# Performance work log

Measured on AMD Instinct MI355X. Metric: run time of the kernel, lower is better.

Reference implementation:

```python
import jax, jax.numpy as jnp
import numpy as np

N_NODES = 50000
N_EDGES = 800000
F_DIM = 64
AVG_D_LOG = 2.833  # avg_d['log'] ~ log(avg_degree + 1)
EPS_STD = 1e-5     # PNA std aggregator epsilon
EPS_BN = 1e-5      # BatchNorm1d epsilon


def setup_inputs() -> dict:
    key = jax.random.key(0)
    k = jax.random.split(key, 5)
    h = jax.random.normal(k[0], (N_NODES, F_DIM), dtype=jnp.float32)
    src = jax.random.randint(k[1], (N_EDGES,), 0, N_NODES)
    dst = jax.random.randint(k[2], (N_EDGES,), 0, N_NODES)
    # posttrans: single Linear(12*F, F) (posttrans_layers=1, last_activation='none')
    W = jax.random.normal(k[3], (12 * F_DIM, F_DIM), dtype=jnp.float32) * 0.02
    b = jnp.zeros((F_DIM,), dtype=jnp.float32)
    gamma = jnp.ones((F_DIM,), dtype=jnp.float32)
    beta = jnp.zeros((F_DIM,), dtype=jnp.float32)
    return {"h": h, "src": src, "dst": dst, "W": W, "b": b, "gamma": gamma, "beta": beta}


def reference(h, src, dst, W, b, gamma, beta):
    N = h.shape[0]
    m = h[src]  # [E, F] messages: copy_u
    ones = jnp.ones((src.shape[0],), dtype=h.dtype)
    deg = jax.ops.segment_sum(ones, dst, num_segments=N)            # [N]
    s = jax.ops.segment_sum(m, dst, num_segments=N)                 # [N, F]
    s2 = jax.ops.segment_sum(m * m, dst, num_segments=N)            # [N, F]
    mx = jax.ops.segment_max(m, dst, num_segments=N)                # [N, F]
    mn = jax.ops.segment_min(m, dst, num_segments=N)                # [N, F]

    degc = jnp.maximum(deg, 1.0)[:, None]
    mean = s / degc
    var = jax.nn.relu(s2 / degc - mean * mean)
    std = jnp.sqrt(var + EPS_STD)

    # aggregator concat (dim=1): [mean | max | min | std] -> [N, 4F]
    agg = jnp.concatenate([mean, mx, mn, std], axis=1)
    has = (deg > 0)[:, None]
    agg = jnp.where(has, agg, 0.0)  # DGL zero-fills zero-in-degree nodes

    logD = jnp.log(deg + 1.0)[:, None]
    amp = agg * (logD / AVG_D_LOG)
    att = agg * jnp.where(has, AVG_D_LOG / jnp.maximum(logD, 1e-12), 0.0)

    # scaler concat: [identity | amplification | attenuation] -> [N, 12F]
    x = jnp.concatenate([agg, amp, att], axis=1)

    # posttrans linear
    x = x @ W + b

    # BatchNorm1d (training-mode batch statistics)
    mu = jnp.mean(x, axis=0)
    v = jnp.var(x, axis=0)
    x = gamma * (x - mu) / jnp.sqrt(v + EPS_BN) + beta

    x = jax.nn.relu(x)
    x = h + x  # residual (in_dim == out_dim)
    # dropout p=0.0 -> identity
    return x
```

## Files before the change

### kernel.cpp

```cpp
#include <hip/hip_runtime.h>
#include <hip/hip_bf16.h>

#define NND 50000
#define NED 800000
#define FD 64
#define PADW 64
#define MPAD2 50176
#define NBLK 196
#define NEBLK 3125
#define NXCD 8
#define NPX 6250
#define AVGDL 2.833f

typedef __attribute__((ext_vector_type(8))) short short8;
typedef __attribute__((ext_vector_type(4))) float floatx4;

__global__ __launch_bounds__(256) void prep(const float* __restrict__ W,
                                            __hip_bfloat16* __restrict__ Wf,
                                            int* __restrict__ deg,
                                            float* __restrict__ gsum,
                                            float* __restrict__ gsumsq,
                                            __hip_bfloat16* __restrict__ aggb) {
    int i = blockIdx.x * 256 + threadIdx.x;
    if (i < NND) deg[i] = 0;
    if (i < 64) { gsum[i] = 0.f; gsumsq[i] = 0.f; }
    if (i < (MPAD2 - NND) * 128) ((unsigned int*)(aggb + (size_t)NND * 256))[i] = 0u;
    if (i < 8 * 12 * 64 * 8) {
        int e = i & 7;
        int l = (i >> 3) & 63;
        int st = i >> 9;
        int t = st % 12, s5 = st / 12;
        int k = 32 * s5 + (l >> 4) * 8 + e;
        int col = 16 * t + (l & 15);
        int g = col >> 6, jj = col & 63;
        Wf[i] = __float2bfloat16(W[(g * 256 + k) * FD + jj]);
    }
}

__global__ __launch_bounds__(256) void fill_csr(const int* __restrict__ src,
                                                const int* __restrict__ dst,
                                                int* __restrict__ deg,
                                                int* __restrict__ csr) {
    int g = blockIdx.x & (NXCD - 1);
    int e = (blockIdx.x >> 3) * 256 + threadIdx.x;
    if (e < NED) {
        int d = dst[e];
        if ((unsigned)(d - g * NPX) < (unsigned)NPX) {
            int slot = atomicAdd(&deg[d], 1);
            if (slot < PADW) csr[d * PADW + slot] = src[e];
        }
    }
}

__global__ __launch_bounds__(256) void aggregate(
    const float* __restrict__ h, const int* __restrict__ deg,
    const int* __restrict__ csr, __hip_bfloat16* __restrict__ aggb,
    float* __restrict__ c1, float* __restrict__ c2) {
    int wid = blockIdx.x * 4 + (threadIdx.x >> 6);
    int lane = threadIdx.x & 63;
    if (wid >= NND) return;
    int d = deg[wid];
    if (d > PADW) d = PADW;
    float s = 0.f, s2 = 0.f, mx = -INFINITY, mn = INFINITY;
    if (d > 0) {
        const int* row_idx = csr + wid * PADW;
        int myidx = row_idx[lane < d ? lane : d - 1];
        for (int j = 0; j < d; j += 8) {
            float vv[8];
            #pragma unroll
            for (int q = 0; q < 8; ++q) {
                int jj = j + q;
                int jc = jj < d ? jj : d - 1;
                int ii = __shfl(myidx, jc);
                vv[q] = h[(size_t)ii * FD + lane];
            }
            #pragma unroll
            for (int q = 0; q < 8; ++q) {
                bool ok = (j + q) < d;
                float v = ok ? vv[q] : 0.f;
                s += v; s2 += v * v;
                mx = fmaxf(mx, ok ? vv[q] : -INFINITY);
                mn = fminf(mn, ok ? vv[q] : INFINITY);
            }
        }
    }
    float mean = 0.f, maxv = 0.f, minv = 0.f, stdv = 0.f, cc1 = 0.f, cc2 = 0.f;
    if (d > 0) {
        float degf = (float)d;
        mean = s / degf;
        float var = fmaxf(s2 / degf - mean * mean, 0.f);
        stdv = sqrtf(var + 1e-5f);
        maxv = mx; minv = mn;
        float logD = logf(degf + 1.f);
        cc1 = logD / AVGDL;
        cc2 = AVGDL / fmaxf(logD, 1e-12f);
    }
    __hip_bfloat16* row = aggb + (size_t)wid * 256;
    row[lane]       = __float2bfloat16(mean);
    row[64 + lane]  = __float2bfloat16(maxv);
    row[128 + lane] = __float2bfloat16(minv);
    row[192 + lane] = __float2bfloat16(stdv);
    if (lane == 0) { c1[wid] = cc1; c2[wid] = cc2; }
}

__global__ __launch_bounds__(512) void gemm_kernel(
    const __hip_bfloat16* __restrict__ aggb, const __hip_bfloat16* __restrict__ Wf,
    const float* __restrict__ c1, const float* __restrict__ c2,
    const float* __restrict__ bias,
    float* __restrict__ x, float* __restrict__ gsum, float* __restrict__ gsumsq) {
    __shared__ short8 Bsm[6144];
    __shared__ float cs[64], css[64];
    int tid = threadIdx.x;
    const short8* Wf8 = (const short8*)Wf;
    #pragma unroll
    for (int i = 0; i < 12; ++i) Bsm[i * 512 + tid] = Wf8[i * 512 + tid];
    if (tid < 64) { cs[tid] = 0.f; css[tid] = 0.f; }
    __syncthreads();

    int w = tid >> 6, lane = tid & 63;
    int c = lane & 15, hi = lane >> 4;
    int rowBase = blockIdx.x * 256 + w * 32;
    const short8* A8 = (const short8*)aggb;

    floatx4 acc[2][12];
    #pragma unroll
    for (int p = 0; p < 2; ++p)
        #pragma unroll
        for (int t = 0; t < 12; ++t) acc[p][t] = (floatx4){0.f, 0.f, 0.f, 0.f};

    #pragma unroll
    for (int s5 = 0; s5 < 8; ++s5) {
        short8 a0 = A8[(size_t)(rowBase + c) * 32 + 4 * s5 + hi];
        short8 a1 = A8[(size_t)(rowBase + 16 + c) * 32 + 4 * s5 + hi];
        #pragma unroll
        for (int t = 0; t < 12; ++t) {
            short8 b = Bsm[(s5 * 12 + t) * 64 + lane];
            acc[0][t] = __builtin_amdgcn_mfma_f32_16x16x32_bf16(a0, b, acc[0][t], 0, 0, 0);
            acc[1][t] = __builtin_amdgcn_mfma_f32_16x16x32_bf16(a1, b, acc[1][t], 0, 0, 0);
        }
    }

    float bv[4];
    #pragma unroll
    for (int t = 0; t < 4; ++t) bv[t] = bias[16 * t + c];
    float psum[4] = {0.f, 0.f, 0.f, 0.f}, psq[4] = {0.f, 0.f, 0.f, 0.f};
    #pragma unroll
    for (int p = 0; p < 2; ++p) {
        #pragma unroll
        for (int r = 0; r < 4; ++r) {
            int row = rowBase + p * 16 + hi * 4 + r;
            bool valid = row < NND;
            float c1v = valid ? c1[row] : 0.f;
            float c2v = valid ? c2[row] : 0.f;
            #pragma unroll
            for (int t = 0; t < 4; ++t) {
                float val = acc[p][t][r] + c1v * acc[p][t + 4][r] + c2v * acc[p][t + 8][r] + bv[t];
                if (valid) {
                    x[(size_t)row * FD + 16 * t + c] = val;
                    psum[t] += val;
                    psq[t] += val * val;
                }
            }
        }
    }
    #pragma unroll
    for (int t = 0; t < 4; ++t) {
        float rs = psum[t], rq = psq[t];
        rs += __shfl_xor(rs, 16); rs += __shfl_xor(rs, 32);
        rq += __shfl_xor(rq, 16); rq += __shfl_xor(rq, 32);
        if (hi == 0) { atomicAdd(&cs[16 * t + c], rs); atomicAdd(&css[16 * t + c], rq); }
    }
    __syncthreads();
    if (tid < 64) { atomicAdd(&gsum[tid], cs[tid]); atomicAdd(&gsumsq[tid], css[tid]); }
}

__global__ __launch_bounds__(256) void finalize(
    const float* __restrict__ x, const float* __restrict__ h,
    const float* __restrict__ gsum, const float* __restrict__ gsumsq,
    const float* __restrict__ gamma, const float* __restrict__ beta,
    float* __restrict__ out) {
    __shared__ float sc[64], sh[64];
    int tid = threadIdx.x;
    if (tid < 64) {
        float mu = gsum[tid] * (1.f / NND);
        float var = gsumsq[tid] * (1.f / NND) - mu * mu;
        float s = gamma[tid] * rsqrtf(var + 1e-5f);
        sc[tid] = s;
        sh[tid] = beta[tid] - mu * s;
    }
    __syncthreads();
    int i = blockIdx.x * 256 + tid;
    if (i >= NND * FD / 4) return;
    int jj = (i & 15) * 4;
    floatx4 xv = ((const floatx4*)x)[i];
    floatx4 hv = ((const floatx4*)h)[i];
    floatx4 o;
    #pragma unroll
    for (int q = 0; q < 4; ++q) {
        float v = sc[jj + q] * xv[q] + sh[jj + q];
        o[q] = hv[q] + fmaxf(v, 0.f);
    }
    ((floatx4*)out)[i] = o;
}

extern "C" void kernel_launch(void* const* d_in, const int* in_sizes, int n_in,
                              void* d_out, int out_size, void* d_ws, size_t ws_size,
                              hipStream_t stream) {
    const float* h     = (const float*)d_in[0];
    const int*   src   = (const int*)d_in[1];
    const int*   dst   = (const int*)d_in[2];
    const float* W     = (const float*)d_in[3];
    const float* bias  = (const float*)d_in[4];
    const float* gamma = (const float*)d_in[5];
    const float* beta  = (const float*)d_in[6];
    float* out = (float*)d_out;

    char* ws = (char*)d_ws;
    size_t off = 0;
    auto alloc = [&](size_t bytes) -> char* {
        char* p = ws + off;
        off = (off + bytes + 255) & ~(size_t)255;
        return p;
    };
    int* deg        = (int*)alloc(NND * 4);
    int* csr        = (int*)alloc((size_t)NND * PADW * 4);
    float* c1       = (float*)alloc(MPAD2 * 4);
    float* c2       = (float*)alloc(MPAD2 * 4);
    __hip_bfloat16* aggb = (__hip_bfloat16*)alloc((size_t)MPAD2 * 256 * 2);
    __hip_bfloat16* Wf   = (__hip_bfloat16*)alloc(8 * 12 * 64 * 8 * 2);
    float* x        = (float*)alloc((size_t)NND * FD * 4);
    float* gsum     = (float*)alloc(64 * 4);
    float* gsumsq   = (float*)alloc(64 * 4);

    prep<<<NBLK, 256, 0, stream>>>(W, Wf, deg, gsum, gsumsq, aggb);
    fill_csr<<<NEBLK * NXCD, 256, 0, stream>>>(src, dst, deg, csr);
    aggregate<<<(NND + 3) / 4, 256, 0, stream>>>(h, deg, csr, aggb, c1, c2);
    gemm_kernel<<<NBLK, 512, 0, stream>>>(aggb, Wf, c1, c2, bias, x, gsum, gsumsq);
    finalize<<<(NND * FD / 4 + 255) / 256, 256, 0, stream>>>(x, h, gsum, gsumsq, gamma, beta, out);
}
```

Measured before the change: 172.4 us.

## Fuse BatchNorm finalize into GEMM via grid-wide atomic barrier

Result: slower. 194.6 us (+12.9%).

```diff
diff --git a/kernel.cpp b/kernel.cpp
--- a/kernel.cpp
+++ b/kernel.cpp
@@ -20,10 +20,12 @@
                                             int* __restrict__ deg,
                                             float* __restrict__ gsum,
                                             float* __restrict__ gsumsq,
-                                            __hip_bfloat16* __restrict__ aggb) {
+                                            __hip_bfloat16* __restrict__ aggb,
+                                            int* __restrict__ bar) {
     int i = blockIdx.x * 256 + threadIdx.x;
     if (i < NND) deg[i] = 0;
     if (i < 64) { gsum[i] = 0.f; gsumsq[i] = 0.f; }
+    if (i == 0) *bar = 0;
     if (i < (MPAD2 - NND) * 128) ((unsigned int*)(aggb + (size_t)NND * 256))[i] = 0u;
     if (i < 8 * 12 * 64 * 8) {
         int e = i & 7;
@@ -103,13 +105,16 @@
     if (lane == 0) { c1[wid] = cc1; c2[wid] = cc2; }
 }
 
-__global__ __launch_bounds__(512) void gemm_kernel(
+__global__ __launch_bounds__(512) void gemm_fused(
     const __hip_bfloat16* __restrict__ aggb, const __hip_bfloat16* __restrict__ Wf,
     const float* __restrict__ c1, const float* __restrict__ c2,
     const float* __restrict__ bias,
-    float* __restrict__ x, float* __restrict__ gsum, float* __restrict__ gsumsq) {
+    const float* __restrict__ h, const float* __restrict__ gamma,
+    const float* __restrict__ beta, float* __restrict__ out,
+    float* __restrict__ gsum, float* __restrict__ gsumsq, int* __restrict__ bar) {
     __shared__ short8 Bsm[6144];
     __shared__ float cs[64], css[64];
+    __shared__ float sc2[64], sh2[64];
     int tid = threadIdx.x;
     const short8* Wf8 = (const short8*)Wf;
     #pragma unroll
@@ -143,6 +148,7 @@
     float bv[4];
     #pragma unroll
     for (int t = 0; t < 4; ++t) bv[t] = bias[16 * t + c];
+    float val[2][4][4];
     float psum[4] = {0.f, 0.f, 0.f, 0.f}, psq[4] = {0.f, 0.f, 0.f, 0.f};
     #pragma unroll
     for (int p = 0; p < 2; ++p) {
@@ -154,12 +160,9 @@
             float c2v = valid ? c2[row] : 0.f;
             #pragma unroll
             for (int t = 0; t < 4; ++t) {
-                float val = acc[p][t][r] + c1v * acc[p][t + 4][r] + c2v * acc[p][t + 8][r] + bv[t];
-                if (valid) {
-                    x[(size_t)row * FD + 16 * t + c] = val;
-                    psum[t] += val;
-                    psq[t] += val * val;
-                }
+                float v = acc[p][t][r] + c1v * acc[p][t + 4][r] + c2v * acc[p][t + 8][r] + bv[t];
+                val[p][r][t] = v;
+                if (valid) { psum[t] += v; psq[t] += v * v; }
             }
         }
     }
@@ -172,35 +175,41 @@
     }
     __syncthreads();
     if (tid < 64) { atomicAdd(&gsum[tid], cs[tid]); atomicAdd(&gsumsq[tid], css[tid]); }
-}
-
-__global__ __launch_bounds__(256) void finalize(
-    const float* __restrict__ x, const float* __restrict__ h,
-    const float* __restrict__ gsum, const float* __restrict__ gsumsq,
-    const float* __restrict__ gamma, const float* __restrict__ beta,
-    float* __restrict__ out) {
-    __shared__ float sc[64], sh[64];
-    int tid = threadIdx.x;
+
+    __threadfence();
+    __syncthreads();
+    if (tid == 0) {
+        __hip_atomic_fetch_add(bar, 1, __ATOMIC_ACQ_REL, __HIP_MEMORY_SCOPE_AGENT);
+        while (__hip_atomic_load(bar, __ATOMIC_ACQUIRE, __HIP_MEMORY_SCOPE_AGENT) < (int)gridDim.x) {}
+    }
+    __syncthreads();
+
     if (tid < 64) {
-        float mu = gsum[tid] * (1.f / NND);
-        float var = gsumsq[tid] * (1.f / NND) - mu * mu;
-        float s = gamma[tid] * rsqrtf(var + 1e-5f);
-        sc[tid] = s;
-        sh[tid] = beta[tid] - mu * s;
-    }
-    __syncthreads();
-    int i = blockIdx.x * 256 + tid;
-    if (i >= NND * FD / 4) return;
-    int jj = (i & 15) * 4;
-    floatx4 xv = ((const floatx4*)x)[i];
-    floatx4 hv = ((const floatx4*)h)[i];
-    floatx4 o;
-    #pragma unroll
-    for (int q = 0; q < 4; ++q) {
-        float v = sc[jj + q] * xv[q] + sh[jj + q];
-        o[q] = hv[q] + fmaxf(v, 0.f);
-    }
-    ((floatx4*)out)[i] = o;
+        float s = __hip_atomic_load(&gsum[tid], __ATOMIC_RELAXED, __HIP_MEMORY_SCOPE_AGENT);
+        float q = __hip_atomic_load(&gsumsq[tid], __ATOMIC_RELAXED, __HIP_MEMORY_SCOPE_AGENT);
+        float mu = s * (1.f / NND);
+        float var = q * (1.f / NND) - mu * mu;
+        float scl = gamma[tid] * rsqrtf(var + 1e-5f);
+        sc2[tid] = scl;
+        sh2[tid] = beta[tid] - mu * scl;
+    }
+    __syncthreads();
+
+    #pragma unroll
+    for (int p = 0; p < 2; ++p) {
+        #pragma unroll
+        for (int r = 0; r < 4; ++r) {
+            int row = rowBase + p * 16 + hi * 4 + r;
+            if (row < NND) {
+                #pragma unroll
+                for (int t = 0; t < 4; ++t) {
+                    int col = 16 * t + c;
+                    float v = sc2[col] * val[p][r][t] + sh2[col];
+                    out[(size_t)row * FD + col] = h[(size_t)row * FD + col] + fmaxf(v, 0.f);
+                }
+            }
+        }
+    }
 }
 
 extern "C" void kernel_launch(void* const* d_in, const int* in_sizes, int n_in,
@@ -228,13 +237,13 @@
     float* c2       = (float*)alloc(MPAD2 * 4);
     __hip_bfloat16* aggb = (__hip_bfloat16*)alloc((size_t)MPAD2 * 256 * 2);
     __hip_bfloat16* Wf   = (__hip_bfloat16*)alloc(8 * 12 * 64 * 8 * 2);
-    float* x        = (float*)alloc((size_t)NND * FD * 4);
     float* gsum     = (float*)alloc(64 * 4);
     float* gsumsq   = (float*)alloc(64 * 4);
-
-    prep<<<NBLK, 256, 0, stream>>>(W, Wf, deg, gsum, gsumsq, aggb);
+    int* bar        = (int*)alloc(4);
+
+    prep<<<NBLK, 256, 0, stream>>>(W, Wf, deg, gsum, gsumsq, aggb, bar);
     fill_csr<<<NEBLK * NXCD, 256, 0, stream>>>(src, dst, deg, csr);
     aggregate<<<(NND + 3) / 4, 256, 0, stream>>>(h, deg, csr, aggb, c1, c2);
-    gemm_kernel<<<NBLK, 512, 0, stream>>>(aggb, Wf, c1, c2, bias, x, gsum, gsumsq);
-    finalize<<<(NND * FD / 4 + 255) / 256, 256, 0, stream>>>(x, h, gsum, gsumsq, gamma, beta, out);
-}
+    gemm_fused<<<NBLK, 512, 0, stream>>>(aggb, Wf, c1, c2, bias, h, gamma, beta,
+                                         out, gsum, gsumsq, bar);
+}
```

## Vectorize neighbor gathers in aggregate with float4 loads and cross-lane reduction

Applied to the files above, without the earlier changes.

After: 174.8 us. Within noise of the previous version (+1.4%).

```diff
diff --git a/kernel.cpp b/kernel.cpp
--- a/kernel.cpp
+++ b/kernel.cpp
@@ -13,6 +13,7 @@
 #define AVGDL 2.833f
 
 typedef __attribute__((ext_vector_type(8))) short short8;
+typedef __attribute__((ext_vector_type(4))) short short4v;
 typedef __attribute__((ext_vector_type(4))) float floatx4;
 
 __global__ __launch_bounds__(256) void prep(const float* __restrict__ W,
@@ -61,45 +62,64 @@
     if (wid >= NND) return;
     int d = deg[wid];
     if (d > PADW) d = PADW;
-    float s = 0.f, s2 = 0.f, mx = -INFINITY, mn = INFINITY;
+    int q = lane & 15, sub = lane >> 4;
+    floatx4 s  = (floatx4){0.f, 0.f, 0.f, 0.f};
+    floatx4 s2 = (floatx4){0.f, 0.f, 0.f, 0.f};
+    floatx4 mx = (floatx4){-INFINITY, -INFINITY, -INFINITY, -INFINITY};
+    floatx4 mn = (floatx4){INFINITY, INFINITY, INFINITY, INFINITY};
     if (d > 0) {
         const int* row_idx = csr + wid * PADW;
         int myidx = row_idx[lane < d ? lane : d - 1];
         for (int j = 0; j < d; j += 8) {
-            float vv[8];
+            int j0 = j + sub, j1 = j + 4 + sub;
+            int jc0 = j0 < d ? j0 : d - 1;
+            int jc1 = j1 < d ? j1 : d - 1;
+            int i0 = __shfl(myidx, jc0);
+            int i1 = __shfl(myidx, jc1);
+            floatx4 v0 = *(const floatx4*)(&h[(size_t)i0 * FD + 4 * q]);
+            floatx4 v1 = *(const floatx4*)(&h[(size_t)i1 * FD + 4 * q]);
+            bool ok0 = j0 < d, ok1 = j1 < d;
             #pragma unroll
-            for (int q = 0; q < 8; ++q) {
-                int jj = j + q;
-                int jc = jj < d ? jj : d - 1;
-                int ii = __shfl(myidx, jc);
-                vv[q] = h[(size_t)ii * FD + lane];
+            for (int k = 0; k < 4; ++k) {
+                float a = ok0 ? v0[k] : 0.f;
+                float b = ok1 ? v1[k] : 0.f;
+                s[k] += a + b;
+                s2[k] += a * a + b * b;
+                mx[k] = fmaxf(mx[k], fmaxf(ok0 ? v0[k] : -INFINITY, ok1 ? v1[k] : -INFINITY));
+                mn[k] = fminf(mn[k], fminf(ok0 ? v0[k] : INFINITY, ok1 ? v1[k] : INFINITY));
             }
-            #pragma unroll
-            for (int q = 0; q < 8; ++q) {
-                bool ok = (j + q) < d;
-                float v = ok ? vv[q] : 0.f;
-                s += v; s2 += v * v;
-                mx = fmaxf(mx, ok ? vv[q] : -INFINITY);
-                mn = fminf(mn, ok ? vv[q] : INFINITY);
-            }
-        }
-    }
-    float mean = 0.f, maxv = 0.f, minv = 0.f, stdv = 0.f, cc1 = 0.f, cc2 = 0.f;
+        }
+    }
+    #pragma unroll
+    for (int m = 16; m <= 32; m <<= 1) {
+        #pragma unroll
+        for (int k = 0; k < 4; ++k) {
+            s[k]  += __shfl_xor(s[k], m);
+            s2[k] += __shfl_xor(s2[k], m);
+            mx[k] = fmaxf(mx[k], __shfl_xor(mx[k], m));
+            mn[k] = fminf(mn[k], __shfl_xor(mn[k], m));
+        }
+    }
+    float cc1 = 0.f, cc2 = 0.f;
+    floatx4 statv = (floatx4){0.f, 0.f, 0.f, 0.f};
     if (d > 0) {
         float degf = (float)d;
-        mean = s / degf;
-        float var = fmaxf(s2 / degf - mean * mean, 0.f);
-        stdv = sqrtf(var + 1e-5f);
-        maxv = mx; minv = mn;
+        float inv = 1.f / degf;
+        #pragma unroll
+        for (int k = 0; k < 4; ++k) {
+            float mean = s[k] * inv;
+            float var = fmaxf(s2[k] * inv - mean * mean, 0.f);
+            float stdv = sqrtf(var + 1e-5f);
+            statv[k] = (sub == 0) ? mean : (sub == 1) ? mx[k] : (sub == 2) ? mn[k] : stdv;
+        }
         float logD = logf(degf + 1.f);
         cc1 = logD / AVGDL;
         cc2 = AVGDL / fmaxf(logD, 1e-12f);
     }
-    __hip_bfloat16* row = aggb + (size_t)wid * 256;
-    row[lane]       = __float2bfloat16(mean);
-    row[64 + lane]  = __float2bfloat16(maxv);
-    row[128 + lane] = __float2bfloat16(minv);
-    row[192 + lane] = __float2bfloat16(stdv);
+    union { __hip_bfloat16 b[4]; short4v v; } u;
+    #pragma unroll
+    for (int k = 0; k < 4; ++k) u.b[k] = __float2bfloat16(statv[k]);
+    *(short4v*)(aggb + (size_t)wid * 256 + sub * 64 + 4 * q) = u.v;
     if (lane == 0) { c1[wid] = cc1; c2[wid] = cc2; }
 }
 
```
